# Performance work log

Hardware: AMD Instinct MI355X
Metric: run time of the kernel (lower is better)

## Reference

```python
import jax, jax.numpy as jnp
import numpy as np

N_NODES = 100000
HIDDEN = 128
N_EDGES = 1000000


def setup_inputs() -> dict:
    key = jax.random.key(0)
    k1, k2, k3, k4 = jax.random.split(key, 4)
    z = jax.random.normal(k1, (N_NODES, HIDDEN), dtype=jnp.float32)
    edge_label_index = jax.random.randint(k2, (2, N_EDGES), 0, N_NODES, dtype=jnp.int64)
    # Kaiming-ish scaled init for the two Linear layers (lin1: 2H->H, lin2: H->1)
    W1 = jax.random.normal(k3, (2 * HIDDEN, HIDDEN), dtype=jnp.float32) / np.sqrt(2 * HIDDEN)
    b1 = jnp.zeros((HIDDEN,), dtype=jnp.float32)
    W2 = jax.random.normal(k4, (HIDDEN, 1), dtype=jnp.float32) / np.sqrt(HIDDEN)
    b2 = jnp.zeros((1,), dtype=jnp.float32)
    return {"z": z, "edge_label_index": edge_label_index, "W1": W1, "b1": b1, "W2": W2, "b2": b2}


def reference(z, edge_label_index, W1, b1, W2, b2):
    row, col = edge_label_index[0], edge_label_index[1]
    # gather endpoint embeddings and concat: [E, 2H]
    h = jnp.concatenate([z[row], z[col]], axis=-1)
    h = jax.nn.relu(h @ W1 + b1)          # [E, H]
    out = h @ W2 + b2                     # [E, 1]
    return out.reshape(-1)
```

## Files before the change

### kernel.cpp

```cpp
#include <hip/hip_runtime.h>
#include <hip/hip_bf16.h>
#include <stdint.h>

#define HIDDEN 128

typedef __attribute__((ext_vector_type(8))) short short8;
typedef __attribute__((ext_vector_type(4))) short short4v;
typedef __attribute__((ext_vector_type(4))) float float4v;

static __device__ __forceinline__ unsigned short f2bf(float f) {
    union { float f; unsigned u; } v; v.f = f;
    unsigned r = (v.u + 0x7FFFu + ((v.u >> 16) & 1u)) >> 16;
    return (unsigned short)r;
}
static __device__ __forceinline__ float bf2f(unsigned short h) {
    union { unsigned u; float f; } v; v.u = ((unsigned)h) << 16;
    return v.f;
}

__global__ void prep_wt(const float* __restrict__ W1, const float* __restrict__ b1,
                        const float* __restrict__ W2,
                        unsigned short* __restrict__ Wt,
                        float* __restrict__ b1p, float* __restrict__ W2p) {
    int idx = blockIdx.x * blockDim.x + threadIdx.x;
    if (idx < 256 * 128) {
        int j = idx >> 7, k = idx & 127;
        float v = (j < 128) ? W1[k * 128 + j] : W1[(128 + k) * 128 + (j - 128)];
        Wt[idx] = f2bf(v);
    }
    if (idx < 128) {
        int m = idx >> 3, tt = idx & 7;
        int jj = tt * 16 + m;
        b1p[idx] = b1[jj];
        W2p[idx] = W2[jj];
    }
}

__global__ __launch_bounds__(256) void node_gemm(
        const float* __restrict__ z, const unsigned short* __restrict__ Wt,
        unsigned short* __restrict__ Q, int n_nodes) {
    int lane = threadIdx.x & 63;
    int wave = threadIdx.x >> 6;
    int m = lane & 15;
    int quad = lane >> 4;
    int blockBase = blockIdx.x * 128;

    short8 b[4][4];
    #pragma unroll
    for (int t = 0; t < 4; ++t) {
        const unsigned short* wp = Wt + (size_t)(wave * 64 + t * 16 + m) * HIDDEN;
        #pragma unroll
        for (int s = 0; s < 4; ++s)
            b[t][s] = *(const short8*)(wp + s * 32 + quad * 8);
    }

    int h   = wave >> 1;
    int pp0 = m * 8 + (wave & 1) * 4;

    #pragma unroll 2
    for (int it = 0; it < 8; ++it) {
        int n0 = blockBase + it * 16;
        int row = n0 + m;

        short8 a[4];
        if (row < n_nodes) {
            const float* zp = z + (size_t)row * HIDDEN;
            #pragma unroll
            for (int s = 0; s < 4; ++s) {
                int k0 = s * 32 + quad * 8;
                float4v z0 = *(const float4v*)(zp + k0);
                float4v z1 = *(const float4v*)(zp + k0 + 4);
                short8 t;
                t[0] = (short)f2bf(z0[0]); t[1] = (short)f2bf(z0[1]);
                t[2] = (short)f2bf(z0[2]); t[3] = (short)f2bf(z0[3]);
                t[4] = (short)f2bf(z1[0]); t[5] = (short)f2bf(z1[1]);
                t[6] = (short)f2bf(z1[2]); t[7] = (short)f2bf(z1[3]);
                a[s] = t;
            }
        } else {
            #pragma unroll
            for (int s = 0; s < 4; ++s) a[s] = (short8)(0);
        }

        float4v acc[4];
        #pragma unroll
        for (int t = 0; t < 4; ++t) acc[t] = (float4v)(0.0f);

        #pragma unroll
        for (int t = 0; t < 4; ++t)
            #pragma unroll
            for (int s = 0; s < 4; ++s)
                acc[t] = __builtin_amdgcn_mfma_f32_16x16x32_bf16(a[s], b[t][s], acc[t], 0, 0, 0);

        #pragma unroll
        for (int r = 0; r < 4; ++r) {
            int node = n0 + quad * 4 + r;
            if (node < n_nodes) {
                short4v pk;
                #pragma unroll
                for (int t = 0; t < 4; ++t) pk[t] = (short)f2bf(acc[t][r]);
                *(short4v*)(Q + (size_t)node * 256 + h * 128 + pp0) = pk;
            }
        }
    }
}

__global__ __launch_bounds__(256) void edge_kernel(
        const int* __restrict__ eli, const unsigned short* __restrict__ Q,
        const float* __restrict__ b1p, const float* __restrict__ W2p,
        const float* __restrict__ b2, float* __restrict__ out, int E) {
    int g      = threadIdx.x >> 4;
    int lane16 = threadIdx.x & 15;
    int j0 = lane16 * 8;

    float4v bA = *(const float4v*)(b1p + j0);
    float4v bB = *(const float4v*)(b1p + j0 + 4);
    float4v wA = *(const float4v*)(W2p + j0);
    float4v wB = *(const float4v*)(W2p + j0 + 4);
    float bias2 = b2[0];

    #pragma unroll
    for (int i = 0; i < 4; ++i) {
        int e = blockIdx.x * 64 + i * 16 + g;
        if (e >= E) continue;
        int r = eli[e];
        int c = eli[E + e];

        short8 u1 = *(const short8*)(Q + (size_t)r * 256 + j0);
        short8 u2 = *(const short8*)(Q + (size_t)c * 256 + 128 + j0);

        float acc = 0.0f;
        #pragma unroll
        for (int k = 0; k < 4; ++k) {
            float v = bf2f((unsigned short)u1[k]) + bf2f((unsigned short)u2[k]) + bA[k];
            v = fmaxf(v, 0.0f);
            acc = fmaf(v, wA[k], acc);
        }
        #pragma unroll
        for (int k = 0; k < 4; ++k) {
            float v = bf2f((unsigned short)u1[4 + k]) + bf2f((unsigned short)u2[4 + k]) + bB[k];
            v = fmaxf(v, 0.0f);
            acc = fmaf(v, wB[k], acc);
        }

        acc += __shfl_xor(acc, 1);
        acc += __shfl_xor(acc, 2);
        acc += __shfl_xor(acc, 4);
        acc += __shfl_xor(acc, 8);

        if (lane16 == 0) out[e] = acc + bias2;
    }
}

extern "C" void kernel_launch(void* const* d_in, const int* in_sizes, int n_in,
                              void* d_out, int out_size, void* d_ws, size_t ws_size,
                              hipStream_t stream) {
    const float* z   = (const float*)d_in[0];
    const int*   eli = (const int*)d_in[1];
    const float* W1  = (const float*)d_in[2];
    const float* b1  = (const float*)d_in[3];
    const float* W2  = (const float*)d_in[4];
    const float* b2  = (const float*)d_in[5];
    int n_nodes = in_sizes[0] / HIDDEN;
    int E       = in_sizes[1] / 2;
    float* out  = (float*)d_out;

    size_t qbytes = (size_t)n_nodes * 256 * 2;
    unsigned short* Q   = (unsigned short*)d_ws;
    unsigned short* Wt  = (unsigned short*)((char*)d_ws + qbytes);
    float*          b1p = (float*)((char*)d_ws + qbytes + 256 * 128 * 2);
    float*          W2p = b1p + 128;

    prep_wt<<<128, 256, 0, stream>>>(W1, b1, W2, Wt, b1p, W2p);

    node_gemm<<<(n_nodes + 127) / 128, 256, 0, stream>>>(z, Wt, Q, n_nodes);

    edge_kernel<<<(E + 63) / 64, 256, 0, stream>>>(eli, Q, b1p, W2p, b2, out, E);
}
```

Before: 193.1 us.

## Prefetch node rows, fold bias into node GEMM, batch edge gathers

The node GEMM now software-pipelines its z loads, reading the next 16-row tile while the current one runs through MFMA. It also folds b1 into the row-side projection before the bf16 store. The edge kernel issues all index loads and then all gather loads for its four edges up front to expose memory-level parallelism, and it decodes bf16 pairs with shifts and masks. bf16 packing uses a perm instruction. Costs are higher register pressure and a small rounding change, since bias is added before quantisation.

Result: slower. 198.6 us (+2.8%).

```diff
diff --git a/kernel.cpp b/kernel.cpp
--- a/kernel.cpp
+++ b/kernel.cpp
@@ -5,17 +5,31 @@
 #define HIDDEN 128
 
 typedef __attribute__((ext_vector_type(8))) short short8;
-typedef __attribute__((ext_vector_type(4))) short short4v;
+typedef __attribute__((ext_vector_type(4))) unsigned uint4v;
 typedef __attribute__((ext_vector_type(4))) float float4v;
+typedef __attribute__((ext_vector_type(2))) float float2v;
+typedef __attribute__((ext_vector_type(2))) unsigned uint2v;
 
 static __device__ __forceinline__ unsigned short f2bf(float f) {
     union { float f; unsigned u; } v; v.f = f;
     unsigned r = (v.u + 0x7FFFu + ((v.u >> 16) & 1u)) >> 16;
     return (unsigned short)r;
 }
-static __device__ __forceinline__ float bf2f(unsigned short h) {
-    union { unsigned u; float f; } v; v.u = ((unsigned)h) << 16;
-    return v.f;
+
+static __device__ __forceinline__ unsigned pack2bf(float f0, float f1) {
+    unsigned u0 = __float_as_uint(f0), u1 = __float_as_uint(f1);
+    u0 = u0 + 0x7FFFu + ((u0 >> 16) & 1u);
+    u1 = u1 + 0x7FFFu + ((u1 >> 16) & 1u);
+    return __builtin_amdgcn_perm(u1, u0, 0x07060302u);
+}
+
+static __device__ __forceinline__ short8 pack8(float4v lo, float4v hi) {
+    uint4v u;
+    u[0] = pack2bf(lo[0], lo[1]);
+    u[1] = pack2bf(lo[2], lo[3]);
+    u[2] = pack2bf(hi[0], hi[1]);
+    u[3] = pack2bf(hi[2], hi[3]);
+    return *(short8*)&u;
 }
 
 __global__ void prep_wt(const float* __restrict__ W1, const float* __restrict__ b1,
@@ -38,6 +52,7 @@
 
 __global__ __launch_bounds__(256) void node_gemm(
         const float* __restrict__ z, const unsigned short* __restrict__ Wt,
+        const float* __restrict__ b1p,
         unsigned short* __restrict__ Q, int n_nodes) {
     int lane = threadIdx.x & 63;
     int wave = threadIdx.x >> 6;
@@ -56,99 +71,125 @@
 
     int h   = wave >> 1;
     int pp0 = m * 8 + (wave & 1) * 4;
-
-    #pragma unroll 2
+    float4v b1v = (float4v)(0.0f);
+    if (h == 0) b1v = *(const float4v*)(b1p + pp0);
+
+    const float* zbase = z + (size_t)(blockBase + m) * HIDDEN + quad * 8;
+
+    float4v raw[8];
+    {
+        bool ok = (blockBase + m) < n_nodes;
+        #pragma unroll
+        for (int s = 0; s < 4; ++s) {
+            raw[2 * s]     = ok ? *(const float4v*)(zbase + s * 32)     : (float4v)(0.0f);
+            raw[2 * s + 1] = ok ? *(const float4v*)(zbase + s * 32 + 4) : (float4v)(0.0f);
+        }
+    }
+
+    #pragma unroll
     for (int it = 0; it < 8; ++it) {
-        int n0 = blockBase + it * 16;
-        int row = n0 + m;
-
-        short8 a[4];
-        if (row < n_nodes) {
-            const float* zp = z + (size_t)row * HIDDEN;
+        float4v nxt[8];
+        if (it < 7) {
+            bool ok = (blockBase + (it + 1) * 16 + m) < n_nodes;
+            const float* zn = zbase + (size_t)(it + 1) * 16 * HIDDEN;
             #pragma unroll
             for (int s = 0; s < 4; ++s) {
-                int k0 = s * 32 + quad * 8;
-                float4v z0 = *(const float4v*)(zp + k0);
-                float4v z1 = *(const float4v*)(zp + k0 + 4);
-                short8 t;
-                t[0] = (short)f2bf(z0[0]); t[1] = (short)f2bf(z0[1]);
-                t[2] = (short)f2bf(z0[2]); t[3] = (short)f2bf(z0[3]);
-                t[4] = (short)f2bf(z1[0]); t[5] = (short)f2bf(z1[1]);
-                t[6] = (short)f2bf(z1[2]); t[7] = (short)f2bf(z1[3]);
-                a[s] = t;
+                nxt[2 * s]     = ok ? *(const float4v*)(zn + s * 32)     : (float4v)(0.0f);
+                nxt[2 * s + 1] = ok ? *(const float4v*)(zn + s * 32 + 4) : (float4v)(0.0f);
             }
-        } else {
-            #pragma unroll
-            for (int s = 0; s < 4; ++s) a[s] = (short8)(0);
-        }
+        }
+
+        short8 a[4];
+        #pragma unroll
+        for (int s = 0; s < 4; ++s) a[s] = pack8(raw[2 * s], raw[2 * s + 1]);
 
         float4v acc[4];
         #pragma unroll
         for (int t = 0; t < 4; ++t) acc[t] = (float4v)(0.0f);
-
         #pragma unroll
         for (int t = 0; t < 4; ++t)
             #pragma unroll
             for (int s = 0; s < 4; ++s)
                 acc[t] = __builtin_amdgcn_mfma_f32_16x16x32_bf16(a[s], b[t][s], acc[t], 0, 0, 0);
 
+        int n0 = blockBase + it * 16;
         #pragma unroll
         for (int r = 0; r < 4; ++r) {
             int node = n0 + quad * 4 + r;
             if (node < n_nodes) {
-                short4v pk;
-                #pragma unroll
-                for (int t = 0; t < 4; ++t) pk[t] = (short)f2bf(acc[t][r]);
-                *(short4v*)(Q + (size_t)node * 256 + h * 128 + pp0) = pk;
+                float v0 = acc[0][r] + b1v[0];
+                float v1 = acc[1][r] + b1v[1];
+                float v2 = acc[2][r] + b1v[2];
+                float v3 = acc[3][r] + b1v[3];
+                uint2v pk;
+                pk[0] = pack2bf(v0, v1);
+                pk[1] = pack2bf(v2, v3);
+                *(uint2v*)(Q + (size_t)node * 256 + h * 128 + pp0) = pk;
             }
+        }
+
+        if (it < 7) {
+            #pragma unroll
+            for (int j = 0; j < 8; ++j) raw[j] = nxt[j];
         }
     }
 }
 
 __global__ __launch_bounds__(256) void edge_kernel(
         const int* __restrict__ eli, const unsigned short* __restrict__ Q,
-        const float* __restrict__ b1p, const float* __restrict__ W2p,
-        const float* __restrict__ b2, float* __restrict__ out, int E) {
+        const float* __restrict__ W2p, const float* __restrict__ b2,
+        float* __restrict__ out, int E) {
     int g      = threadIdx.x >> 4;
     int lane16 = threadIdx.x & 15;
     int j0 = lane16 * 8;
 
-    float4v bA = *(const float4v*)(b1p + j0);
-    float4v bB = *(const float4v*)(b1p + j0 + 4);
-    float4v wA = *(const float4v*)(W2p + j0);
-    float4v wB = *(const float4v*)(W2p + j0 + 4);
+    float2v w[4];
+    #pragma unroll
+    for (int k = 0; k < 4; ++k) w[k] = ((const float2v*)(W2p + j0))[k];
     float bias2 = b2[0];
 
+    int e0 = blockIdx.x * 64 + g;
+
+    int idx_r[4], idx_c[4];
     #pragma unroll
     for (int i = 0; i < 4; ++i) {
-        int e = blockIdx.x * 64 + i * 16 + g;
-        if (e >= E) continue;
-        int r = eli[e];
-        int c = eli[E + e];
-
-        short8 u1 = *(const short8*)(Q + (size_t)r * 256 + j0);
-        short8 u2 = *(const short8*)(Q + (size_t)c * 256 + 128 + j0);
-
-        float acc = 0.0f;
+        int e = e0 + i * 16;
+        idx_r[i] = (e < E) ? eli[e]     : 0;
+        idx_c[i] = (e < E) ? eli[E + e] : 0;
+    }
+
+    uint4v u1[4], u2[4];
+    #pragma unroll
+    for (int i = 0; i < 4; ++i) {
+        u1[i] = *(const uint4v*)(Q + (size_t)idx_r[i] * 256 + j0);
+        u2[i] = *(const uint4v*)(Q + (size_t)idx_c[i] * 256 + 128 + j0);
+    }
+
+    #pragma unroll
+    for (int i = 0; i < 4; ++i) {
+        float2v accv = (float2v)(0.0f);
         #pragma unroll
         for (int k = 0; k < 4; ++k) {
-            float v = bf2f((unsigned short)u1[k]) + bf2f((unsigned short)u2[k]) + bA[k];
-            v = fmaxf(v, 0.0f);
-            acc = fmaf(v, wA[k], acc);
-        }
-        #pragma unroll
-        for (int k = 0; k < 4; ++k) {
-            float v = bf2f((unsigned short)u1[4 + k]) + bf2f((unsigned short)u2[4 + k]) + bB[k];
-            v = fmaxf(v, 0.0f);
-            acc = fmaf(v, wB[k], acc);
-        }
-
+            unsigned a1 = u1[i][k], a2 = u2[i][k];
+            float2v v1, v2;
+            v1[0] = __uint_as_float(a1 << 16);
+            v1[1] = __uint_as_float(a1 & 0xFFFF0000u);
+            v2[0] = __uint_as_float(a2 << 16);
+            v2[1] = __uint_as_float(a2 & 0xFFFF0000u);
+            float2v s = v1 + v2;
+            s[0] = fmaxf(s[0], 0.0f);
+            s[1] = fmaxf(s[1], 0.0f);
+            accv[0] = fmaf(s[0], w[k][0], accv[0]);
+            accv[1] = fmaf(s[1], w[k][1], accv[1]);
+        }
+        float acc = accv[0] + accv[1];
         acc += __shfl_xor(acc, 1);
         acc += __shfl_xor(acc, 2);
         acc += __shfl_xor(acc, 4);
         acc += __shfl_xor(acc, 8);
 
-        if (lane16 == 0) out[e] = acc + bias2;
+        int e = e0 + i * 16;
+        if (lane16 == 0 && e < E) out[e] = acc + bias2;
     }
 }
 
@@ -173,7 +214,7 @@
 
     prep_wt<<<128, 256, 0, stream>>>(W1, b1, W2, Wt, b1p, W2p);
 
-    node_gemm<<<(n_nodes + 127) / 128, 256, 0, stream>>>(z, Wt, Q, n_nodes);
-
-    edge_kernel<<<(E + 63) / 64, 256, 0, stream>>>(eli, Q, b1p, W2p, b2, out, E);
-}
+    node_gemm<<<(n_nodes + 127) / 128, 256, 0, stream>>>(z, Wt, b1p, Q, n_nodes);
+
+    edge_kernel<<<(E + 63) / 64, 256, 0, stream>>>(eli, Q, W2p, b2, out, E);
+}
```
